# Optimization experiments

Measured on AMD Instinct MI355X. Metric: run time of the kernel, lower is better.

The kernel has to match this reference:

```python
import jax, jax.numpy as jnp
import numpy as np

B, S, D_IN, D_OUT = 4, 2048, 1024, 1024
N_TREES, DEPTH, N_HEADS = 12, 3, 3
N_INTERNAL = 2 ** DEPTH - 1  # 7
N_LEAVES = 2 ** DEPTH        # 8
TEMPERATURE = 1.0
SOFTPLUS_SHIFT = 0.5413      # softplus(0.5413) ~= 1.0, so init node temp ~ 1


def _build_path_indices(depth):
    """Root-to-leaf internal-node indices and go-left directions per leaf."""
    L = 2 ** depth
    pi = np.zeros((L, depth), np.int32)
    pd = np.zeros((L, depth), np.float32)
    for leaf in range(L):
        node = 0
        for d in range(depth):
            pi[leaf, d] = node
            bit = (leaf >> (depth - 1 - d)) & 1
            pd[leaf, d] = 1.0 - bit
            node = 2 * node + 1 + bit
    return pi, pd


def setup_inputs() -> dict:
    key = jax.random.key(0)
    ks = jax.random.split(key, 4)
    x = jax.random.normal(ks[0], (B, S, D_IN), dtype=jnp.float32)
    # normal(0, 0.1) routing init
    decision_weights = 0.1 * jax.random.normal(ks[1], (N_TREES, N_INTERNAL, D_IN), dtype=jnp.float32)
    decision_biases = jnp.zeros((N_TREES, N_INTERNAL), dtype=jnp.float32)
    node_temperature_logits = jnp.zeros((N_TREES, N_INTERNAL), dtype=jnp.float32)
    # nn.Linear default init ~ U(-1/sqrt(D), 1/sqrt(D)); use matching-scale normal
    gate_w = jax.random.normal(ks[2], (N_TREES, D_IN), dtype=jnp.float32) / np.sqrt(D_IN)
    gate_b = jnp.zeros((N_TREES,), dtype=jnp.float32)
    # xavier_normal over each [n_leaves, output_dim] slice
    xav_std = np.sqrt(2.0 / (N_LEAVES + D_OUT))
    leaf_outputs = xav_std * jax.random.normal(ks[3], (N_HEADS, N_TREES, N_LEAVES, D_OUT), dtype=jnp.float32)
    pi, pd = _build_path_indices(DEPTH)
    return {
        "x": x,
        "decision_weights": decision_weights,
        "decision_biases": decision_biases,
        "node_temperature_logits": node_temperature_logits,
        "gate_w": gate_w,
        "gate_b": gate_b,
        "leaf_outputs": leaf_outputs,
        "path_indices": jnp.asarray(pi),
        "path_dirs": jnp.asarray(pd),
    }


def reference(x, decision_weights, decision_biases, node_temperature_logits,
              gate_w, gate_b, leaf_outputs, path_indices, path_dirs):
    # decisions: [B, S, T, N_internal]
    decisions = jnp.einsum('bsd,tnd->bstn', x, decision_weights) + decision_biases
    node_temps = TEMPERATURE * jax.nn.softplus(node_temperature_logits + SOFTPLUS_SHIFT)
    decisions = jax.nn.sigmoid(decisions / node_temps)
    # gather nodes along each root->leaf path: [B, S, T, L, depth]
    relevant = decisions[..., path_indices]
    probs_per_level = path_dirs * relevant + (1.0 - path_dirs) * (1.0 - relevant)
    leaf_probs = probs_per_level.prod(axis=-1)  # [B, S, T, L]
    # softmax gate over trees: [B, S, T]
    weights = jax.nn.softmax(jnp.einsum('bsd,td->bst', x, gate_w) + gate_b, axis=-1)
    # fold tree gate into leaf probs, then contract leaves against leaf outputs
    routed = leaf_probs * weights[..., None]            # [B, S, T, L]
    out = jnp.einsum('bstl,htld->hbsd', routed, leaf_outputs)  # [H, B, S, Dout]
    return out
```

## Files before the change

### kernel.cpp

```cpp
#include <hip/hip_runtime.h>

typedef __attribute__((ext_vector_type(8))) short short8;
typedef __attribute__((ext_vector_type(4))) float floatx4;
typedef unsigned int uint;
typedef unsigned short ushort;
typedef __attribute__((ext_vector_type(4))) uint uintx4;

#define NTOK   8192
#define DIN    1024
#define DOUT   1024
#define NJ     96
#define TOKPB  32
#define XSTR   136
#define DSTR   97
#define SSTR   85
#define LOT_H  (DOUT * NJ)

static __device__ inline ushort f2b(float f) {
    uint u = __builtin_bit_cast(uint, f);
    u = u + 0x7fffu + ((u >> 16) & 1u);
    return (ushort)(u >> 16);
}
static __device__ inline uint pack2(float a, float b) {
    return (uint)f2b(a) | ((uint)f2b(b) << 16);
}

__global__ __launch_bounds__(256) void k_prep(const float* __restrict__ lo,
                                              const float* __restrict__ dw,
                                              const float* __restrict__ gw,
                                              ushort* __restrict__ lot,
                                              ushort* __restrict__ wcat) {
    int i = blockIdx.x * 256 + threadIdx.x;
    if (i < 3 * LOT_H) {
        int h = i / LOT_H;
        int rem = i - h * LOT_H;
        int k = rem >> 10;
        int d = rem & 1023;
        lot[h * LOT_H + d * NJ + k] = f2b(lo[i]);
    } else {
        int j = i - 3 * LOT_H;
        int r = j >> 10, c = j & 1023;
        float v = (r < 84) ? dw[r * DIN + c] : gw[(r - 84) * DIN + c];
        wcat[j] = f2b(v);
    }
}

__global__ __launch_bounds__(256) void k_routed(
    const float* __restrict__ x,
    const ushort* __restrict__ wcat,
    const float* __restrict__ db,
    const float* __restrict__ ntl,
    const float* __restrict__ gb,
    const int*   __restrict__ pi,
    const float* __restrict__ pd,
    ushort* __restrict__ routed)
{
    __shared__ __attribute__((aligned(16))) char smem[34816];
    __shared__ float invt[84];
    __shared__ float biasf[96];
    __shared__ int   pis[24];
    __shared__ float pds[24];

    ushort* xl = (ushort*)smem;
    ushort* wl = (ushort*)(smem + TOKPB * XSTR * 2);
    float*  decis = (float*)smem;
    float*  sdecs = (float*)(smem + TOKPB * DSTR * 4);

    const int tid = threadIdx.x;
    const int tb  = blockIdx.x * TOKPB;

    if (tid < 84) {
        float z = ntl[tid] + 0.5413f;
        float sp = (z > 20.0f) ? z : log1pf(__expf(z));
        invt[tid]  = 1.0f / sp;
        biasf[tid] = db[tid];
    } else if (tid < 96) {
        biasf[tid] = gb[tid - 84];
    } else if (tid < 120) {
        pis[tid - 96] = pi[tid - 96];
    } else if (tid < 144) {
        pds[tid - 120] = pd[tid - 120];
    }

    const int wave = tid >> 6, lane = tid & 63;
    const int lrow = lane & 15, quad = lane >> 4;
    const int wm = wave & 1, wn = wave >> 1;

    floatx4 acc[3];
#pragma unroll
    for (int nt = 0; nt < 3; ++nt) acc[nt] = (floatx4)(0.0f);

    floatx4 xv[2][4];
    uintx4  wv[2][6];

#define LOADX(B, KC) do { \
    _Pragma("unroll") for (int i_ = 0; i_ < 4; ++i_) { \
        int idx_ = tid + 256 * i_; \
        int r_ = idx_ >> 5, c_ = idx_ & 31; \
        xv[B][i_] = __builtin_nontemporal_load( \
            (const floatx4*)(x + (size_t)(tb + r_) * DIN + (KC) * 128 + c_ * 4)); \
    } } while (0)

#define LOADW(B, KC) do { \
    _Pragma("unroll") for (int i_ = 0; i_ < 6; ++i_) { \
        int idx_ = tid + 256 * i_; \
        int r_ = idx_ >> 4, c_ = idx_ & 15; \
        wv[B][i_] = *(const uintx4*)(wcat + r_ * DIN + (KC) * 128 + c_ * 8); \
    } } while (0)

#define STAGE(B) do { \
    _Pragma("unroll") for (int i_ = 0; i_ < 4; ++i_) { \
        int idx_ = tid + 256 * i_; \
        int r_ = idx_ >> 5, c_ = idx_ & 31; \
        uint2 p_; \
        p_.x = pack2(xv[B][i_][0], xv[B][i_][1]); \
        p_.y = pack2(xv[B][i_][2], xv[B][i_][3]); \
        *(uint2*)(xl + r_ * XSTR + c_ * 4) = p_; \
    } \
    _Pragma("unroll") for (int i_ = 0; i_ < 6; ++i_) { \
        int idx_ = tid + 256 * i_; \
        int r_ = idx_ >> 4, c_ = idx_ & 15; \
        *(uintx4*)(wl + r_ * XSTR + c_ * 8) = wv[B][i_]; \
    } } while (0)

    LOADX(0, 0);
    LOADW(0, 0);

#pragma unroll
    for (int kc = 0; kc < 8; ++kc) {
        const int cur = kc & 1, nxt = cur ^ 1;
        __syncthreads();
        STAGE(cur);
        __syncthreads();
        if (kc < 7) {
            LOADX(nxt, kc + 1);
            LOADW(nxt, kc + 1);
        }

        short8 a[4];
#pragma unroll
        for (int kt = 0; kt < 4; ++kt)
            a[kt] = *(const short8*)(xl + (wm * 16 + lrow) * XSTR + kt * 32 + quad * 8);
#pragma unroll
        for (int nt = 0; nt < 3; ++nt) {
#pragma unroll
            for (int kt = 0; kt < 4; ++kt) {
                short8 b = *(const short8*)(wl + (wn * 48 + nt * 16 + lrow) * XSTR + kt * 32 + quad * 8);
                acc[nt] = __builtin_amdgcn_mfma_f32_16x16x32_bf16(a[kt], b, acc[nt], 0, 0, 0);
            }
        }
    }
#undef LOADX
#undef LOADW
#undef STAGE

    __syncthreads();
#pragma unroll
    for (int nt = 0; nt < 3; ++nt)
#pragma unroll
        for (int r = 0; r < 4; ++r)
            decis[(wm * 16 + quad * 4 + r) * DSTR + wn * 48 + nt * 16 + lrow] = acc[nt][r];
    __syncthreads();

#pragma unroll
    for (int i = 0; i < 11; ++i) {
        int idx = tid + 256 * i;
        if (idx < TOKPB * 84) {
            int tk = idx / 84, nd = idx - tk * 84;
            float dv = (decis[tk * DSTR + nd] + biasf[nd]) * invt[nd];
            sdecs[tk * SSTR + nd] = 1.0f / (1.0f + __expf(-dv));
        }
    }
    __syncthreads();

    {
        const int tk = tid >> 3, l = tid & 7;
        float g[12], gm = -1e30f;
#pragma unroll
        for (int tt = 0; tt < 12; ++tt) {
            g[tt] = decis[tk * DSTR + 84 + tt] + biasf[84 + tt];
            gm = fmaxf(gm, g[tt]);
        }
        float gs = 0.0f;
#pragma unroll
        for (int tt = 0; tt < 12; ++tt) { g[tt] = __expf(g[tt] - gm); gs += g[tt]; }
        float ginv = 1.0f / gs;

        const int   n0 = pis[l * 3 + 0], n1 = pis[l * 3 + 1], n2 = pis[l * 3 + 2];
        const float d0 = pds[l * 3 + 0], d1 = pds[l * 3 + 1], d2 = pds[l * 3 + 2];
        const float* sd = sdecs + tk * SSTR;
        ushort* dst = routed + (size_t)(tb + tk) * NJ + l;
#pragma unroll
        for (int t = 0; t < 12; ++t) {
            float s0 = sd[t * 7 + n0], s1 = sd[t * 7 + n1], s2 = sd[t * 7 + n2];
            float pb = g[t] * ginv
                     * (d0 * s0 + (1.0f - d0) * (1.0f - s0))
                     * (d1 * s1 + (1.0f - d1) * (1.0f - s1))
                     * (d2 * s2 + (1.0f - d2) * (1.0f - s2));
            dst[t * 8] = f2b(pb);
        }
    }
}

__global__ __launch_bounds__(256) void k_out(
    const ushort* __restrict__ routed,
    const ushort* __restrict__ lot,
    float* __restrict__ out)
{
    const int tb = blockIdx.x * 64;
    const int d0 = blockIdx.y * 128;
    const int h  = blockIdx.z;
    const int wave = threadIdx.x >> 6, lane = threadIdx.x & 63;
    const int lrow = lane & 15, quad = lane >> 4;

    const ushort* ap = routed + (size_t)(tb + wave * 16 + lrow) * NJ + quad * 8;
    short8 a[3];
#pragma unroll
    for (int kk = 0; kk < 3; ++kk) a[kk] = *(const short8*)(ap + kk * 32);

    const ushort* bp = lot + (size_t)h * LOT_H + (size_t)(d0 + lrow) * NJ + quad * 8;
    floatx4 acc[8];
#pragma unroll
    for (int nt = 0; nt < 8; ++nt) {
        acc[nt] = (floatx4)(0.0f);
#pragma unroll
        for (int kk = 0; kk < 3; ++kk) {
            short8 b = *(const short8*)(bp + nt * 16 * NJ + kk * 32);
            acc[nt] = __builtin_amdgcn_mfma_f32_16x16x32_bf16(a[kk], b, acc[nt], 0, 0, 0);
        }
    }
#pragma unroll
    for (int nt = 0; nt < 8; ++nt) {
        int d = d0 + nt * 16 + lrow;
#pragma unroll
        for (int r = 0; r < 4; ++r) {
            int tok = tb + wave * 16 + quad * 4 + r;
            __builtin_nontemporal_store(acc[nt][r],
                out + ((size_t)h * NTOK + tok) * DOUT + d);
        }
    }
}

extern "C" void kernel_launch(void* const* d_in, const int* in_sizes, int n_in,
                              void* d_out, int out_size, void* d_ws, size_t ws_size,
                              hipStream_t stream) {
    const float* x   = (const float*)d_in[0];
    const float* dw  = (const float*)d_in[1];
    const float* db  = (const float*)d_in[2];
    const float* ntl = (const float*)d_in[3];
    const float* gw  = (const float*)d_in[4];
    const float* gb  = (const float*)d_in[5];
    const float* lo  = (const float*)d_in[6];
    const int*   pi  = (const int*)d_in[7];
    const float* pd  = (const float*)d_in[8];
    float* out = (float*)d_out;

    ushort* routed = (ushort*)d_ws;
    ushort* lot    = routed + (size_t)NTOK * NJ;
    ushort* wcat   = lot + (size_t)3 * LOT_H;

    k_prep<<<dim3((3 * LOT_H + NJ * DIN) / 256), dim3(256), 0, stream>>>(lo, dw, gw, lot, wcat);
    k_routed<<<dim3(NTOK / TOKPB), dim3(256), 0, stream>>>(x, wcat, db, ntl, gb, pi, pd, routed);
    k_out<<<dim3(NTOK / 64, DOUT / 128, 3), dim3(256), 0, stream>>>(routed, lot, out);
}
```

Measured before the change: 174.1 us.

## Fuse routing and leaf-output GEMM into one kernel via shared memory

Merges the routing kernel and the output kernel: routed leaf probabilities stay in LDS as bf16 and each block of 32 tokens computes all 3x1024 outputs directly, with each wave covering 768 output columns. This removes the global round-trip of the routed matrix and one kernel launch. In exchange there are only 256 blocks for the large output write phase, each wave loops over 48 column tiles reading leaf-output rows from L2, and extra LDS lowers occupancy.

Result: faster. 161.1 us (-7.5%).

```diff
diff --git a/kernel.cpp b/kernel.cpp
--- a/kernel.cpp
+++ b/kernel.cpp
@@ -14,6 +14,7 @@
 #define XSTR   136
 #define DSTR   97
 #define SSTR   85
+#define RSTR   104
 #define LOT_H  (DOUT * NJ)
 
 static __device__ inline ushort f2b(float f) {
@@ -45,7 +46,7 @@
     }
 }
 
-__global__ __launch_bounds__(256) void k_routed(
+__global__ __launch_bounds__(256) void k_fused(
     const float* __restrict__ x,
     const ushort* __restrict__ wcat,
     const float* __restrict__ db,
@@ -53,9 +54,11 @@
     const float* __restrict__ gb,
     const int*   __restrict__ pi,
     const float* __restrict__ pd,
-    ushort* __restrict__ routed)
+    const ushort* __restrict__ lot,
+    float* __restrict__ out)
 {
     __shared__ __attribute__((aligned(16))) char smem[34816];
+    __shared__ __attribute__((aligned(16))) ushort rt[TOKPB][RSTR];
     __shared__ float invt[84];
     __shared__ float biasf[96];
     __shared__ int   pis[24];
@@ -189,7 +192,6 @@
         const int   n0 = pis[l * 3 + 0], n1 = pis[l * 3 + 1], n2 = pis[l * 3 + 2];
         const float d0 = pds[l * 3 + 0], d1 = pds[l * 3 + 1], d2 = pds[l * 3 + 2];
         const float* sd = sdecs + tk * SSTR;
-        ushort* dst = routed + (size_t)(tb + tk) * NJ + l;
 #pragma unroll
         for (int t = 0; t < 12; ++t) {
             float s0 = sd[t * 7 + n0], s1 = sd[t * 7 + n1], s2 = sd[t * 7 + n2];
@@ -197,46 +199,37 @@
                      * (d0 * s0 + (1.0f - d0) * (1.0f - s0))
                      * (d1 * s1 + (1.0f - d1) * (1.0f - s1))
                      * (d2 * s2 + (1.0f - d2) * (1.0f - s2));
-            dst[t * 8] = f2b(pb);
-        }
-    }
-}
-
-__global__ __launch_bounds__(256) void k_out(
-    const ushort* __restrict__ routed,
-    const ushort* __restrict__ lot,
-    float* __restrict__ out)
-{
-    const int tb = blockIdx.x * 64;
-    const int d0 = blockIdx.y * 128;
-    const int h  = blockIdx.z;
-    const int wave = threadIdx.x >> 6, lane = threadIdx.x & 63;
-    const int lrow = lane & 15, quad = lane >> 4;
-
-    const ushort* ap = routed + (size_t)(tb + wave * 16 + lrow) * NJ + quad * 8;
-    short8 a[3];
-#pragma unroll
-    for (int kk = 0; kk < 3; ++kk) a[kk] = *(const short8*)(ap + kk * 32);
-
-    const ushort* bp = lot + (size_t)h * LOT_H + (size_t)(d0 + lrow) * NJ + quad * 8;
-    floatx4 acc[8];
-#pragma unroll
-    for (int nt = 0; nt < 8; ++nt) {
-        acc[nt] = (floatx4)(0.0f);
+            rt[tk][t * 8 + l] = f2b(pb);
+        }
+    }
+    __syncthreads();
+
+    {
+        short8 a0[3], a1[3];
 #pragma unroll
         for (int kk = 0; kk < 3; ++kk) {
-            short8 b = *(const short8*)(bp + nt * 16 * NJ + kk * 32);
-            acc[nt] = __builtin_amdgcn_mfma_f32_16x16x32_bf16(a[kk], b, acc[nt], 0, 0, 0);
-        }
-    }
-#pragma unroll
-    for (int nt = 0; nt < 8; ++nt) {
-        int d = d0 + nt * 16 + lrow;
-#pragma unroll
-        for (int r = 0; r < 4; ++r) {
-            int tok = tb + wave * 16 + quad * 4 + r;
-            __builtin_nontemporal_store(acc[nt][r],
-                out + ((size_t)h * NTOK + tok) * DOUT + d);
+            a0[kk] = *(const short8*)(&rt[lrow][quad * 8 + kk * 32]);
+            a1[kk] = *(const short8*)(&rt[16 + lrow][quad * 8 + kk * 32]);
+        }
+#pragma unroll 4
+        for (int nt = 0; nt < 48; ++nt) {
+            int c = wave * 768 + nt * 16;
+            int h = c >> 10;
+            int d = (c & 1023) + lrow;
+            const ushort* bp = lot + (size_t)h * LOT_H + (size_t)d * NJ + quad * 8;
+            floatx4 c0 = (floatx4)(0.0f), c1 = (floatx4)(0.0f);
+#pragma unroll
+            for (int kk = 0; kk < 3; ++kk) {
+                short8 b = *(const short8*)(bp + kk * 32);
+                c0 = __builtin_amdgcn_mfma_f32_16x16x32_bf16(a0[kk], b, c0, 0, 0, 0);
+                c1 = __builtin_amdgcn_mfma_f32_16x16x32_bf16(a1[kk], b, c1, 0, 0, 0);
+            }
+            float* ob = out + ((size_t)h * NTOK + tb) * DOUT + d;
+#pragma unroll
+            for (int r = 0; r < 4; ++r) {
+                __builtin_nontemporal_store(c0[r], ob + (size_t)(quad * 4 + r) * DOUT);
+                __builtin_nontemporal_store(c1[r], ob + (size_t)(16 + quad * 4 + r) * DOUT);
+            }
         }
     }
 }
@@ -255,11 +248,9 @@
     const float* pd  = (const float*)d_in[8];
     float* out = (float*)d_out;
 
-    ushort* routed = (ushort*)d_ws;
-    ushort* lot    = routed + (size_t)NTOK * NJ;
-    ushort* wcat   = lot + (size_t)3 * LOT_H;
+    ushort* lot  = (ushort*)d_ws;
+    ushort* wcat = lot + (size_t)3 * LOT_H;
 
     k_prep<<<dim3((3 * LOT_H + NJ * DIN) / 256), dim3(256), 0, stream>>>(lo, dw, gw, lot, wcat);
-    k_routed<<<dim3(NTOK / TOKPB), dim3(256), 0, stream>>>(x, wcat, db, ntl, gb, pi, pd, routed);
-    k_out<<<dim3(NTOK / 64, DOUT / 128, 3), dim3(256), 0, stream>>>(routed, lot, out);
-}
+    k_fused<<<dim3(NTOK / TOKPB), dim3(256), 0, stream>>>(x, wcat, db, ntl, gb, pi, pd, lot, out);
+}
```
